# Performance work log

Measured on AMD Instinct MI355X. Metric: run time of the kernel, lower is better.

Reference implementation:

```python
import jax, jax.numpy as jnp
import numpy as np

DIM = 192
STATE = 64
B = 8
H = 64
W = 64
EPS_LN = 1e-5
EPS_BN = 1e-5


def _layernorm(x, g, b):
    m = jnp.mean(x, axis=-1, keepdims=True)
    v = jnp.mean((x - m) ** 2, axis=-1, keepdims=True)
    return (x - m) / jnp.sqrt(v + EPS_LN) * g + b


def _linear(x, w, b=None):
    # torch Linear convention: w is [out, in]
    y = jnp.einsum('...i,oi->...o', x, w)
    return y if b is None else y + b


def _parallel_scan(A, Bd, xp):
    # A, Bd, xp: [B, L, S]; h_t = A_t*h_{t-1} + Bd_t*xp_t via log-space cumsum
    A_safe = jnp.clip(A, 0.001, 0.999)
    log_A = jnp.log(A_safe + 1e-10)
    log_cum_A = jnp.cumsum(log_A, axis=1)
    log_cum_A_max = jnp.max(log_cum_A, axis=1, keepdims=True)
    cum_A = jnp.exp(log_cum_A - log_cum_A_max)
    BX = Bd * xp
    # prepend zeros, drop last: normalizer uses cumprod up to t-1
    log_pad = jnp.pad(log_cum_A - log_cum_A_max, ((0, 0), (1, 0), (0, 0)))[:, :-1]
    BX_norm = BX * jnp.exp(-log_pad)
    return jnp.cumsum(BX_norm, axis=1) * cum_A


def _ssm(x, ln_g, ln_b, xp_w, xp_b, dt_w, dt_b, A_log, B_w, C_w, Dp, out_w, out_b):
    xn = _layernorm(x, ln_g, ln_b)
    delta = jax.nn.softplus(_linear(xn, dt_w, dt_b)) * 0.01 + 0.0001  # [B,L,S]
    B_t = _linear(xn, B_w)
    C_t = _linear(xn, C_w)
    A = -jnp.exp(A_log)  # [S]
    x_proj = _linear(xn, xp_w, xp_b)
    deltaA = jnp.clip(delta * A, -10.0, -0.0001)
    A_disc = jnp.exp(deltaA)
    B_disc = delta * B_t
    h = _parallel_scan(A_disc, B_disc, x_proj)
    y = C_t * h
    y = jnp.where(jnp.all(jnp.isfinite(y)), y, jnp.zeros_like(y))
    y = _linear(y, out_w, out_b)
    return y + jnp.clip(Dp, -2.0, 2.0) * x


def reference(x, ln1_g, ln1_b, ln2_g, ln2_b, dw_w, bn_g, bn_b, bn_rm, bn_rv,
              ssm_ln_g, ssm_ln_b, xp_w, xp_b, dt_w, dt_b, A_log, B_w, C_w,
              D_param, out_w, out_b, mlp_w1, mlp_b1, mlp_w2, mlp_b2,
              alpha_local, alpha_ssm, alpha_mlp):
    identity = x
    # depthwise 3x3 conv + BatchNorm2d (eval mode, running stats)
    xc = jax.lax.conv_general_dilated(
        x, dw_w, (1, 1), 'SAME', feature_group_count=DIM,
        dimension_numbers=('NCHW', 'OIHW', 'NCHW'))
    scale = (bn_g / jnp.sqrt(bn_rv + EPS_BN))[None, :, None, None]
    x_local = (xc - bn_rm[None, :, None, None]) * scale + bn_b[None, :, None, None]
    # SSM branch on flattened spatial sequence
    x_seq = x.transpose(0, 2, 3, 1).reshape(B, H * W, DIM)
    x_seq = _layernorm(x_seq, ln1_g, ln1_b)
    x_seq = _ssm(x_seq, ssm_ln_g, ssm_ln_b, xp_w, xp_b, dt_w, dt_b, A_log,
                 B_w, C_w, D_param, out_w, out_b)
    x_ssm = x_seq.reshape(B, H, W, DIM).transpose(0, 3, 1, 2)
    xr = identity + alpha_local * x_local + alpha_ssm * x_ssm
    # residual MLP (dropout = identity at inference)
    x_mlp = xr.transpose(0, 2, 3, 1).reshape(B, H * W, DIM)
    x_mlp = _layernorm(x_mlp, ln2_g, ln2_b)
    x_mlp = _linear(jax.nn.gelu(_linear(x_mlp, mlp_w1, mlp_b1), approximate=False),
                    mlp_w2, mlp_b2)
    return xr + alpha_mlp * x_mlp.reshape(B, H, W, DIM).transpose(0, 3, 1, 2)


def setup_inputs() -> dict:
    key = jax.random.key(0)
    ks = jax.random.split(key, 12)
    def nrm(k, shape, s):
        return jax.random.normal(k, shape, jnp.float32) * s
    f32 = jnp.float32
    return {
        'x': jax.random.normal(ks[0], (B, DIM, H, W), f32),
        'ln1_g': jnp.ones(DIM, f32), 'ln1_b': jnp.zeros(DIM, f32),
        'ln2_g': jnp.ones(DIM, f32), 'ln2_b': jnp.zeros(DIM, f32),
        'dw_w': nrm(ks[1], (DIM, 1, 3, 3), 0.2),
        'bn_g': jnp.ones(DIM, f32), 'bn_b': jnp.zeros(DIM, f32),
        'bn_rm': jnp.zeros(DIM, f32), 'bn_rv': jnp.ones(DIM, f32),
        'ssm_ln_g': jnp.ones(DIM, f32), 'ssm_ln_b': jnp.zeros(DIM, f32),
        'xp_w': nrm(ks[2], (STATE, DIM), 0.05), 'xp_b': jnp.zeros(STATE, f32),
        'dt_w': nrm(ks[3], (STATE, DIM), 0.05), 'dt_b': jnp.zeros(STATE, f32),
        'A_log': jnp.log(jax.random.uniform(ks[4], (STATE,), f32) * 0.8 + 0.2),
        'B_w': nrm(ks[5], (STATE, DIM), 0.05),
        'C_w': nrm(ks[6], (STATE, DIM), 0.05),
        'D_param': jnp.zeros(DIM, f32),
        'out_w': nrm(ks[7], (DIM, STATE), 0.05), 'out_b': jnp.zeros(DIM, f32),
        'mlp_w1': nrm(ks[8], (4 * DIM, DIM), 0.03), 'mlp_b1': jnp.zeros(4 * DIM, f32),
        'mlp_w2': nrm(ks[9], (DIM, 4 * DIM), 0.03), 'mlp_b2': jnp.zeros(DIM, f32),
        'alpha_local': jnp.full((1,), 0.5, f32),
        'alpha_ssm': jnp.full((1,), 0.5, f32),
        'alpha_mlp': jnp.full((1,), 0.5, f32),
    }
```

## Files before the change

kernel.cpp:

```cpp
#include <hip/hip_runtime.h>
#include <hip/hip_bf16.h>
#include <math.h>


#define DEV static __device__ __forceinline__

constexpr int Bn = 8, Dm = 192, Ln = 4096, Sn = 64, Hd = 768;

typedef __attribute__((ext_vector_type(8))) short bf16x8;
typedef __attribute__((ext_vector_type(4))) float f32x4;

DEV float wave_sum(float v) {
#pragma unroll
  for (int off = 1; off < 64; off <<= 1) v += __shfl_xor(v, off);
  return v;
}

DEV short f2b(float x) {
  __hip_bfloat16 h = __float2bfloat16(x);
  return *(short*)&h;
}

DEV float b2f(short x) {
  __hip_bfloat16 h = *(__hip_bfloat16*)&x;
  return __bfloat162float(h);
}

__global__ __launch_bounds__(256) void k_prep(
    const float* __restrict__ x, const float* __restrict__ g1, const float* __restrict__ b1,
    const float* __restrict__ g2, const float* __restrict__ b2,
    short* __restrict__ xnb, short* __restrict__ xln1b,
    const float* __restrict__ dt_w, const float* __restrict__ B_w,
    const float* __restrict__ C_w, const float* __restrict__ xp_w,
    const float* __restrict__ out_w, const float* __restrict__ w1,
    const float* __restrict__ w2, short* __restrict__ wb) {
  __shared__ __align__(16) float tile[Dm * 65];
  int tid = threadIdx.x;
  if (blockIdx.y == 8) {
    for (int i = blockIdx.x * 256 + tid; i < 89088; i += 64 * 256) {
      const float4* src;
      if (i < 3072)       src = (const float4*)dt_w + i;
      else if (i < 6144)  src = (const float4*)B_w + (i - 3072);
      else if (i < 9216)  src = (const float4*)C_w + (i - 6144);
      else if (i < 12288) src = (const float4*)xp_w + (i - 9216);
      else if (i < 15360) src = (const float4*)out_w + (i - 12288);
      else if (i < 52224) src = (const float4*)w1 + (i - 15360);
      else                src = (const float4*)w2 + (i - 52224);
      float4 v = *src;
      int o = i * 4;
      wb[o] = f2b(v.x); wb[o + 1] = f2b(v.y); wb[o + 2] = f2b(v.z); wb[o + 3] = f2b(v.w);
    }
    return;
  }
  int b = blockIdx.y, l0 = blockIdx.x * 64;
  const float* xb = x + (size_t)b * Dm * Ln;
  for (int i = tid; i < Dm * 16; i += 256) {
    int d = i >> 4, l4 = (i & 15) << 2;
    float4 v = *(const float4*)&xb[d * Ln + l0 + l4];
    tile[d * 65 + l4]     = v.x; tile[d * 65 + l4 + 1] = v.y;
    tile[d * 65 + l4 + 2] = v.z; tile[d * 65 + l4 + 3] = v.w;
  }
  __syncthreads();
  int lane = tid & 63, wv = tid >> 6;
  float ga0 = g1[lane], ga1 = g1[lane + 64], ga2 = g1[lane + 128];
  float bb0 = b1[lane], bb1 = b1[lane + 64], bb2 = b1[lane + 128];
  float gc0 = g2[lane], gc1 = g2[lane + 64], gc2 = g2[lane + 128];
  float bc0 = b2[lane], bc1 = b2[lane + 64], bc2 = b2[lane + 128];
  for (int li = wv; li < 64; li += 4) {
    float v0 = tile[lane * 65 + li], v1 = tile[(lane + 64) * 65 + li], v2 = tile[(lane + 128) * 65 + li];
    float s  = wave_sum(v0 + v1 + v2);
    float sq = wave_sum(v0 * v0 + v1 * v1 + v2 * v2);
    float m = s * (1.f / 192.f);
    float inv = rsqrtf(sq * (1.f / 192.f) - m * m + 1e-5f);
    float y0 = (v0 - m) * inv * ga0 + bb0;
    float y1 = (v1 - m) * inv * ga1 + bb1;
    float y2 = (v2 - m) * inv * ga2 + bb2;
    float s2  = wave_sum(y0 + y1 + y2);
    float sq2 = wave_sum(y0 * y0 + y1 * y1 + y2 * y2);
    float m2 = s2 * (1.f / 192.f);
    float inv2 = rsqrtf(sq2 * (1.f / 192.f) - m2 * m2 + 1e-5f);
    size_t base = ((size_t)b * Ln + l0 + li) * Dm;
    xln1b[base + lane]       = f2b(y0);
    xln1b[base + lane + 64]  = f2b(y1);
    xln1b[base + lane + 128] = f2b(y2);
    xnb[base + lane]       = f2b((y0 - m2) * inv2 * gc0 + bc0);
    xnb[base + lane + 64]  = f2b((y1 - m2) * inv2 * gc1 + bc1);
    xnb[base + lane + 128] = f2b((y2 - m2) * inv2 * gc2 + bc2);
  }
}

__global__ __launch_bounds__(256) void k_proj(
    const short* __restrict__ xnb, const short* __restrict__ wcat,
    const float* __restrict__ dt_b, const float* __restrict__ xp_b,
    const float* __restrict__ A_log, float* __restrict__ aA, unsigned* __restrict__ bxc) {
  __shared__ __align__(16) short As[64 * 72];
  __shared__ __align__(16) short Bs[256 * 72];
  int m0 = blockIdx.x * 64, tid = threadIdx.x;
  int lane = tid & 63, l16 = lane & 15, quad = lane >> 4, w = tid >> 6;
  f32x4 acc[16] = {};
  for (int kt = 0; kt < 3; kt++) {
    int kb = kt * 64;
    for (int i = tid; i < 512; i += 256) {
      int row = i >> 3, c8 = (i & 7) * 8;
      *(float4*)&As[row * 72 + c8] = *(const float4*)&xnb[(size_t)(m0 + row) * 192 + kb + c8];
    }
    for (int i = tid; i < 2048; i += 256) {
      int row = i >> 3, c8 = (i & 7) * 8;
      *(float4*)&Bs[row * 72 + c8] = *(const float4*)&wcat[(size_t)row * 192 + kb + c8];
    }
    __syncthreads();
#pragma unroll
    for (int ks = 0; ks < 2; ks++) {
      int ko = ks * 32 + quad * 8;
      bf16x8 a0 = *(const bf16x8*)&As[(w * 16 + l16) * 72 + ko];
#pragma unroll
      for (int nh = 0; nh < 2; nh++) {
        bf16x8 bfr[8];
#pragma unroll
        for (int j = 0; j < 8; j++) bfr[j] = *(const bf16x8*)&Bs[((nh * 8 + j) * 16 + l16) * 72 + ko];
#pragma unroll
        for (int j = 0; j < 8; j++)
          acc[nh * 8 + j] = __builtin_amdgcn_mfma_f32_16x16x32_bf16(a0, bfr[j], acc[nh * 8 + j], 0, 0, 0);
      }
    }
    __syncthreads();
  }
  float Av[4], dtbv[4], xpbv[4];
#pragma unroll
  for (int ni = 0; ni < 4; ni++) {
    int s = ni * 16 + l16;
    Av[ni] = -expf(A_log[s]); dtbv[ni] = dt_b[s]; xpbv[ni] = xp_b[s];
  }
#pragma unroll
  for (int r = 0; r < 4; r++) {
    int m = m0 + w * 16 + quad * 4 + r;
#pragma unroll
    for (int ni = 0; ni < 4; ni++) {
      int s = ni * 16 + l16;
      float z = acc[ni][r] + dtbv[ni];
      float sp = (z > 20.f) ? z : log1pf(expf(z));
      float delta = sp * 0.01f + 0.0001f;
      float bt  = acc[ni + 4][r];
      float ct  = acc[ni + 8][r];
      float xpv = acc[ni + 12][r] + xpbv[ni];
      float dA = fminf(fmaxf(delta * Av[ni], -10.f), -0.0001f);
      float Ae = fminf(fmaxf(expf(dA), 0.001f), 0.999f) + 1e-10f;
      aA[(size_t)m * 64 + s] = Ae;
      unsigned pk = (unsigned)(unsigned short)f2b(delta * bt * xpv)
                  | ((unsigned)(unsigned short)f2b(ct) << 16);
      bxc[(size_t)m * 64 + s] = pk;
    }
  }
}

__global__ __launch_bounds__(64) void k_scan1(const float* __restrict__ aA,
                                              const unsigned* __restrict__ bxc,
                                              float* __restrict__ sums) {
  int c = blockIdx.x, b = blockIdx.y, s = threadIdx.x;
  size_t r0 = (size_t)b * Ln + c * 32;
  const float* ap = aA + r0 * 64;
  const unsigned* bp = bxc + r0 * 64;
  float prodA = 1.f, h = 0.f;
  int t = 0;
  if (c == 0) { prodA = ap[s]; h = b2f((short)(bp[s] & 0xFFFF)); t = 1; }
#pragma unroll 4
  for (; t < 32; t++) {
    float a = ap[t * 64 + s];
    float bx = b2f((short)(bp[t * 64 + s] & 0xFFFF));
    h = a * (h + bx);
    prodA *= a;
  }
  int ci = b * 128 + c;
  sums[(ci * 2 + 0) * 64 + s] = prodA;
  sums[(ci * 2 + 1) * 64 + s] = h;
}

__global__ __launch_bounds__(64) void k_scan2(const float* __restrict__ sums, float* __restrict__ carries) {
  int b = blockIdx.x, s = threadIdx.x;
  float cur = 0.f;
#pragma unroll 4
  for (int c = 0; c < 128; c++) {
    int ci = b * 128 + c;
    carries[ci * 64 + s] = cur;
    cur = sums[(ci * 2 + 0) * 64 + s] * cur + sums[(ci * 2 + 1) * 64 + s];
  }
}

__global__ __launch_bounds__(64) void k_scan3(const float* __restrict__ aA,
                                              const unsigned* __restrict__ bxc,
                                              const float* __restrict__ carries,
                                              short* __restrict__ y) {
  int c = blockIdx.x, b = blockIdx.y, s = threadIdx.x;
  size_t r0 = (size_t)b * Ln + c * 32;
  const float* ap = aA + r0 * 64;
  const unsigned* bp = bxc + r0 * 64;
  short* yo = y + r0 * 64;
  float h = carries[(b * 128 + c) * 64 + s];
  int t = 0;
  if (c == 0) {
    unsigned u = bp[s];
    h = b2f((short)(u & 0xFFFF));
    yo[s] = f2b(b2f((short)(u >> 16)) * h);
    t = 1;
  }
#pragma unroll 4
  for (; t < 32; t++) {
    unsigned u = bp[t * 64 + s];
    float a = ap[t * 64 + s];
    h = a * (h + b2f((short)(u & 0xFFFF)));
    yo[t * 64 + s] = f2b(b2f((short)(u >> 16)) * h);
  }
}

__global__ __launch_bounds__(256) void k_out(
    const short* __restrict__ y, const short* __restrict__ owb, const float* __restrict__ out_b,
    const float* __restrict__ Dp, const short* __restrict__ xln1b, float* __restrict__ sout) {
  __shared__ __align__(16) short As[96 * 72];
  __shared__ __align__(16) short Bs[64 * 72];
  int l0g = blockIdx.x * 64, d0 = blockIdx.y * 96, tid = threadIdx.x;
  int lane = tid & 63, l16 = lane & 15, quad = lane >> 4;
  int wm = (tid >> 6) >> 1, wn = (tid >> 6) & 1;
  f32x4 acc[3][2] = {};
  for (int i = tid; i < 768; i += 256) {
    int row = i >> 3, c8 = (i & 7) * 8;
    *(float4*)&As[row * 72 + c8] = *(const float4*)&owb[(d0 + row) * 64 + c8];
  }
  for (int i = tid; i < 512; i += 256) {
    int row = i >> 3, c8 = (i & 7) * 8;
    *(float4*)&Bs[row * 72 + c8] = *(const float4*)&y[(size_t)(l0g + row) * 64 + c8];
  }
  __syncthreads();
#pragma unroll
  for (int ks = 0; ks < 2; ks++) {
    int ko = ks * 32 + quad * 8;
    bf16x8 a[3], b[2];
#pragma unroll
    for (int mi = 0; mi < 3; mi++) a[mi] = *(const bf16x8*)&As[(wm * 48 + mi * 16 + l16) * 72 + ko];
#pragma unroll
    for (int ni = 0; ni < 2; ni++) b[ni] = *(const bf16x8*)&Bs[(wn * 32 + ni * 16 + l16) * 72 + ko];
#pragma unroll
    for (int mi = 0; mi < 3; mi++)
#pragma unroll
      for (int ni = 0; ni < 2; ni++)
        acc[mi][ni] = __builtin_amdgcn_mfma_f32_16x16x32_bf16(a[mi], b[ni], acc[mi][ni], 0, 0, 0);
  }
  int bb = l0g >> 12;
#pragma unroll
  for (int mi = 0; mi < 3; mi++)
#pragma unroll
    for (int r = 0; r < 4; r++) {
      int d = d0 + wm * 48 + mi * 16 + quad * 4 + r;
      float ob = out_b[d];
      float dc = fminf(fmaxf(Dp[d], -2.f), 2.f);
#pragma unroll
      for (int ni = 0; ni < 2; ni++) {
        int l = l0g + wn * 32 + ni * 16 + l16;
        float v = acc[mi][ni][r] + ob;
        if (dc != 0.f) v += dc * b2f(xln1b[(size_t)l * 192 + d]);
        sout[((size_t)bb * Dm + d) * Ln + (l & 4095)] = v;
      }
    }
}

__global__ __launch_bounds__(256) void k_conv(
    const float* __restrict__ x, const float* __restrict__ dw,
    const float* __restrict__ bn_g, const float* __restrict__ bn_b,
    const float* __restrict__ bn_rm, const float* __restrict__ bn_rv,
    const float* __restrict__ sout, const float* __restrict__ a_loc,
    const float* __restrict__ a_ssm, float* __restrict__ xr) {
  __shared__ __align__(16) float xs[64 * 64];
  int d = blockIdx.x, b = blockIdx.y, tid = threadIdx.x;
  const float* xp = x + ((size_t)b * Dm + d) * Ln;
  for (int i = tid; i < 1024; i += 256) ((float4*)xs)[i] = ((const float4*)xp)[i];
  __syncthreads();
  float w[9];
#pragma unroll
  for (int k = 0; k < 9; k++) w[k] = dw[d * 9 + k];
  float scale = bn_g[d] * rsqrtf(bn_rv[d] + 1e-5f);
  float rm = bn_rm[d], bb = bn_b[d];
  float al = a_loc[0], as_ = a_ssm[0];
  const float* sp = sout + ((size_t)b * Dm + d) * Ln;
  float* xo = xr + ((size_t)b * Dm + d) * Ln;
  for (int i = tid; i < 4096; i += 256) {
    int h = i >> 6, wc = i & 63;
    float acc = 0.f;
#pragma unroll
    for (int kh = 0; kh < 3; kh++) {
      int hh = h + kh - 1;
      if (hh < 0 || hh >= 64) continue;
#pragma unroll
      for (int kw = 0; kw < 3; kw++) {
        int ww2 = wc + kw - 1;
        if (ww2 < 0 || ww2 >= 64) continue;
        acc += xs[hh * 64 + ww2] * w[kh * 3 + kw];
      }
    }
    float xl = (acc - rm) * scale + bb;
    xo[i] = xs[i] + al * xl + as_ * sp[i];
  }
}

__global__ __launch_bounds__(256) void k_ln2(
    const float* __restrict__ xr, const float* __restrict__ g, const float* __restrict__ bb,
    short* __restrict__ xn2) {
  __shared__ __align__(16) float tile[Dm * 65];
  int b = blockIdx.y, l0 = blockIdx.x * 64, tid = threadIdx.x;
  const float* xb = xr + (size_t)b * Dm * Ln;
  for (int i = tid; i < Dm * 16; i += 256) {
    int d = i >> 4, l4 = (i & 15) << 2;
    float4 v = *(const float4*)&xb[d * Ln + l0 + l4];
    tile[d * 65 + l4]     = v.x; tile[d * 65 + l4 + 1] = v.y;
    tile[d * 65 + l4 + 2] = v.z; tile[d * 65 + l4 + 3] = v.w;
  }
  __syncthreads();
  int lane = tid & 63, wv = tid >> 6;
  float g0 = g[lane], g1v = g[lane + 64], g2v = g[lane + 128];
  float b0 = bb[lane], b1v = bb[lane + 64], b2v = bb[lane + 128];
  for (int li = wv; li < 64; li += 4) {
    float v0 = tile[lane * 65 + li], v1 = tile[(lane + 64) * 65 + li], v2 = tile[(lane + 128) * 65 + li];
    float s  = wave_sum(v0 + v1 + v2);
    float sq = wave_sum(v0 * v0 + v1 * v1 + v2 * v2);
    float m = s * (1.f / 192.f);
    float inv = rsqrtf(sq * (1.f / 192.f) - m * m + 1e-5f);
    size_t base = ((size_t)b * Ln + l0 + li) * Dm;
    xn2[base + lane]       = f2b((v0 - m) * inv * g0 + b0);
    xn2[base + lane + 64]  = f2b((v1 - m) * inv * g1v + b1v);
    xn2[base + lane + 128] = f2b((v2 - m) * inv * g2v + b2v);
  }
}

__global__ __launch_bounds__(256) void k_gemm1(
    const short* __restrict__ xn2, const short* __restrict__ w1b,
    const float* __restrict__ b1h, short* __restrict__ hid) {
  __shared__ __align__(16) short smem[2 * 128 * 88];
  short* As = smem;
  short* Bs = smem + 128 * 88;
  int m0 = blockIdx.x * 128, n0 = blockIdx.y * 128, tid = threadIdx.x;
  int lane = tid & 63, l16 = lane & 15, quad = lane >> 4;
  int wm = (tid >> 6) >> 1, wn = (tid >> 6) & 1;
  f32x4 acc[4][4] = {};
  for (int kt = 0; kt < 3; kt++) {
    int kb = kt * 64;
    for (int i = tid; i < 1024; i += 256) {
      int row = i >> 3, c8 = (i & 7) * 8;
      *(float4*)&As[row * 88 + c8] = *(const float4*)&xn2[(size_t)(m0 + row) * 192 + kb + c8];
      *(float4*)&Bs[row * 88 + c8] = *(const float4*)&w1b[(size_t)(n0 + row) * 192 + kb + c8];
    }
    __syncthreads();
#pragma unroll
    for (int ks = 0; ks < 2; ks++) {
      int ko = ks * 32 + quad * 8;
      bf16x8 a[4], b[4];
#pragma unroll
      for (int mi = 0; mi < 4; mi++) a[mi] = *(const bf16x8*)&As[(wm * 64 + mi * 16 + l16) * 88 + ko];
#pragma unroll
      for (int ni = 0; ni < 4; ni++) b[ni] = *(const bf16x8*)&Bs[(wn * 64 + ni * 16 + l16) * 88 + ko];
#pragma unroll
      for (int mi = 0; mi < 4; mi++)
#pragma unroll
        for (int ni = 0; ni < 4; ni++)
          acc[mi][ni] = __builtin_amdgcn_mfma_f32_16x16x32_bf16(a[mi], b[ni], acc[mi][ni], 0, 0, 0);
    }
    __syncthreads();
  }
  short* Cs = smem;
  float bias4[4];
#pragma unroll
  for (int ni = 0; ni < 4; ni++) bias4[ni] = b1h[n0 + wn * 64 + ni * 16 + l16];
#pragma unroll
  for (int mi = 0; mi < 4; mi++)
#pragma unroll
    for (int ni = 0; ni < 4; ni++) {
      int n = wn * 64 + ni * 16 + l16;
#pragma unroll
      for (int r = 0; r < 4; r++) {
        int m = wm * 64 + mi * 16 + quad * 4 + r;
        float v = acc[mi][ni][r] + bias4[ni];
        float g = 0.5f * v * (1.f + erff(v * 0.70710678118f));
        Cs[m * 136 + n] = f2b(g);
      }
    }
  __syncthreads();
  for (int i = tid; i < 2048; i += 256) {
    int m = i >> 4, ch = i & 15;
    *(float4*)&hid[(size_t)(m0 + m) * 768 + n0 + ch * 8] = *(const float4*)&Cs[m * 136 + ch * 8];
  }
}

__global__ __launch_bounds__(256) void k_gemm2(
    const short* __restrict__ hid, const short* __restrict__ w2b,
    const float* __restrict__ b2o, const float* __restrict__ xr,
    const float* __restrict__ am, float* __restrict__ out) {
  __shared__ __align__(16) short Wt[96 * 88];
  __shared__ __align__(16) short Ht[64 * 88];
  int l0g = blockIdx.x * 64, d0 = blockIdx.y * 96, tid = threadIdx.x;
  int lane = tid & 63, l16 = lane & 15, quad = lane >> 4;
  int wm = (tid >> 6) >> 1, wn = (tid >> 6) & 1;
  f32x4 acc[3][2] = {};
  for (int kt = 0; kt < 12; kt++) {
    int kb = kt * 64;
    for (int i = tid; i < 768; i += 256) {
      int row = i >> 3, c8 = (i & 7) * 8;
      *(float4*)&Wt[row * 88 + c8] = *(const float4*)&w2b[(size_t)(d0 + row) * 768 + kb + c8];
    }
    for (int i = tid; i < 512; i += 256) {
      int row = i >> 3, c8 = (i & 7) * 8;
      *(float4*)&Ht[row * 88 + c8] = *(const float4*)&hid[(size_t)(l0g + row) * 768 + kb + c8];
    }
    __syncthreads();
#pragma unroll
    for (int ks = 0; ks < 2; ks++) {
      int ko = ks * 32 + quad * 8;
      bf16x8 a[3], b[2];
#pragma unroll
      for (int mi = 0; mi < 3; mi++) a[mi] = *(const bf16x8*)&Wt[(wm * 48 + mi * 16 + l16) * 88 + ko];
#pragma unroll
      for (int ni = 0; ni < 2; ni++) b[ni] = *(const bf16x8*)&Ht[(wn * 32 + ni * 16 + l16) * 88 + ko];
#pragma unroll
      for (int mi = 0; mi < 3; mi++)
#pragma unroll
        for (int ni = 0; ni < 2; ni++)
          acc[mi][ni] = __builtin_amdgcn_mfma_f32_16x16x32_bf16(a[mi], b[ni], acc[mi][ni], 0, 0, 0);
    }
    __syncthreads();
  }
  float alpha = am[0];
#pragma unroll
  for (int mi = 0; mi < 3; mi++)
#pragma unroll
    for (int r = 0; r < 4; r++) {
      int d = d0 + wm * 48 + mi * 16 + quad * 4 + r;
      float bias = b2o[d];
#pragma unroll
      for (int ni = 0; ni < 2; ni++) {
        int lg = l0g + wn * 32 + ni * 16 + l16;
        size_t idx = ((size_t)(lg >> 12) * Dm + d) * Ln + (lg & 4095);
        out[idx] = xr[idx] + alpha * (acc[mi][ni][r] + bias);
      }
    }
}

extern "C" void kernel_launch(void* const* d_in, const int* in_sizes, int n_in,
                              void* d_out, int out_size, void* d_ws, size_t ws_size,
                              hipStream_t stream) {
  (void)in_sizes; (void)n_in; (void)out_size; (void)ws_size;
  const float* x     = (const float*)d_in[0];
  const float* ln1_g = (const float*)d_in[1];
  const float* ln1_b = (const float*)d_in[2];
  const float* ln2_g = (const float*)d_in[3];
  const float* ln2_b = (const float*)d_in[4];
  const float* dw_w  = (const float*)d_in[5];
  const float* bn_g  = (const float*)d_in[6];
  const float* bn_b  = (const float*)d_in[7];
  const float* bn_rm = (const float*)d_in[8];
  const float* bn_rv = (const float*)d_in[9];
  const float* ssm_g = (const float*)d_in[10];
  const float* ssm_b = (const float*)d_in[11];
  const float* xp_w  = (const float*)d_in[12];
  const float* xp_b  = (const float*)d_in[13];
  const float* dt_w  = (const float*)d_in[14];
  const float* dt_b  = (const float*)d_in[15];
  const float* A_log = (const float*)d_in[16];
  const float* B_w   = (const float*)d_in[17];
  const float* C_w   = (const float*)d_in[18];
  const float* Dp    = (const float*)d_in[19];
  const float* out_w = (const float*)d_in[20];
  const float* out_b = (const float*)d_in[21];
  const float* w1    = (const float*)d_in[22];
  const float* b1    = (const float*)d_in[23];
  const float* w2    = (const float*)d_in[24];
  const float* b2    = (const float*)d_in[25];
  const float* a_loc = (const float*)d_in[26];
  const float* a_ssm = (const float*)d_in[27];
  const float* a_mlp = (const float*)d_in[28];

  float* ws = (float*)d_ws;
  short*    xnb   = (short*)ws;
  short*    xln1b = (short*)(ws + 3145728);
  float*    aA    = ws + 6291456;
  unsigned* bxc   = (unsigned*)(ws + 8388608);
  short*    yB    = (short*)(ws + 10485760);
  float*    sout  = ws + 11534336;
  float*    xr    = ws + 17825792;
  short*    wb    = (short*)(ws + 24117248);
  float*    sums  = ws + 24829952;
  float*    carr  = ws + 24961024;
  short*    xn2   = (short*)(ws + 25026560);
  short*    hid   = (short*)(ws + 28172288);
  short*    wcatb = wb;
  short*    owb   = wb + 49152;
  short*    w1b   = wb + 61440;
  short*    w2b   = wb + 208896;
  float*    out   = (float*)d_out;

  k_prep <<<dim3(64, 9),  256, 0, stream>>>(x, ln1_g, ln1_b, ssm_g, ssm_b, xnb, xln1b,
                                            dt_w, B_w, C_w, xp_w, out_w, w1, w2, wb);
  k_proj <<<dim3(512),    256, 0, stream>>>(xnb, wcatb, dt_b, xp_b, A_log, aA, bxc);
  k_scan1<<<dim3(128, 8),  64, 0, stream>>>(aA, bxc, sums);
  k_scan2<<<dim3(8),       64, 0, stream>>>(sums, carr);
  k_scan3<<<dim3(128, 8),  64, 0, stream>>>(aA, bxc, carr, yB);
  k_out  <<<dim3(512, 2), 256, 0, stream>>>(yB, owb, out_b, Dp, xln1b, sout);
  k_conv <<<dim3(192, 8), 256, 0, stream>>>(x, dw_w, bn_g, bn_b, bn_rm, bn_rv, sout, a_loc, a_ssm, xr);
  k_ln2  <<<dim3(64, 8),  256, 0, stream>>>(xr, ln2_g, ln2_b, xn2);
  k_gemm1<<<dim3(256, 6), 256, 0, stream>>>(xn2, w1b, b1, hid);
  k_gemm2<<<dim3(512, 2), 256, 0, stream>>>(hid, w2b, b2, xr, a_mlp, out);
}
```

Baseline: 290.2 us.

## Fuse SSM output projection with depthwise conv and residual combine

Merges the out-projection GEMM kernel and the depthwise conv/BN/residual kernel into one kernel. After the MFMA tile, each block stages a 3-row halo of x (bf16) plus per-channel conv/BN parameters in shared memory, computes the conv per output element, and writes xr directly. This removes the fp32 sout intermediate round-trip and one launch. It adds bf16 rounding of the conv input and scattered strided x reads, and the larger shared footprint may lower occupancy.

After: 307.9 us. 6.1% more time.

```diff
diff --git a/kernel.cpp b/kernel.cpp
--- a/kernel.cpp
+++ b/kernel.cpp
@@ -212,12 +212,21 @@
   }
 }
 
-__global__ __launch_bounds__(256) void k_out(
+__global__ __launch_bounds__(256) void k_outconv(
     const short* __restrict__ y, const short* __restrict__ owb, const float* __restrict__ out_b,
-    const float* __restrict__ Dp, const short* __restrict__ xln1b, float* __restrict__ sout) {
-  __shared__ __align__(16) short As[96 * 72];
-  __shared__ __align__(16) short Bs[64 * 72];
+    const float* __restrict__ Dp, const short* __restrict__ xln1b,
+    const float* __restrict__ x, const float* __restrict__ dw,
+    const float* __restrict__ bn_g, const float* __restrict__ bn_b,
+    const float* __restrict__ bn_rm, const float* __restrict__ bn_rv,
+    const float* __restrict__ a_loc, const float* __restrict__ a_ssm,
+    float* __restrict__ xr) {
+  __shared__ __align__(16) short smem[22080];
+  short* As = smem;
+  short* Bs = smem + 6912;
+  short* xl = smem;
+  float* prm = (float*)(smem + 19008);
   int l0g = blockIdx.x * 64, d0 = blockIdx.y * 96, tid = threadIdx.x;
+  int b = l0g >> 12, h = (l0g >> 6) & 63;
   int lane = tid & 63, l16 = lane & 15, quad = lane >> 4;
   int wm = (tid >> 6) >> 1, wn = (tid >> 6) & 1;
   f32x4 acc[3][2] = {};
@@ -233,71 +242,70 @@
 #pragma unroll
   for (int ks = 0; ks < 2; ks++) {
     int ko = ks * 32 + quad * 8;
-    bf16x8 a[3], b[2];
+    bf16x8 a[3], bfr[2];
 #pragma unroll
     for (int mi = 0; mi < 3; mi++) a[mi] = *(const bf16x8*)&As[(wm * 48 + mi * 16 + l16) * 72 + ko];
 #pragma unroll
-    for (int ni = 0; ni < 2; ni++) b[ni] = *(const bf16x8*)&Bs[(wn * 32 + ni * 16 + l16) * 72 + ko];
+    for (int ni = 0; ni < 2; ni++) bfr[ni] = *(const bf16x8*)&Bs[(wn * 32 + ni * 16 + l16) * 72 + ko];
 #pragma unroll
     for (int mi = 0; mi < 3; mi++)
 #pragma unroll
       for (int ni = 0; ni < 2; ni++)
-        acc[mi][ni] = __builtin_amdgcn_mfma_f32_16x16x32_bf16(a[mi], b[ni], acc[mi][ni], 0, 0, 0);
-  }
-  int bb = l0g >> 12;
+        acc[mi][ni] = __builtin_amdgcn_mfma_f32_16x16x32_bf16(a[mi], bfr[ni], acc[mi][ni], 0, 0, 0);
+  }
+  __syncthreads();
+  for (int i = tid; i < 4608; i += 256) {
+    int rr = i / 1536, rem = i % 1536;
+    int d = rem >> 4, w4 = (rem & 15) * 4;
+    int hh = h - 1 + rr;
+    float4 v = make_float4(0.f, 0.f, 0.f, 0.f);
+    if (hh >= 0 && hh < 64)
+      v = *(const float4*)&x[((size_t)b * Dm + d0 + d) * Ln + hh * 64 + w4];
+    int o = rr * 6336 + d * 66 + 1 + w4;
+    xl[o] = f2b(v.x); xl[o + 1] = f2b(v.y); xl[o + 2] = f2b(v.z); xl[o + 3] = f2b(v.w);
+  }
+  for (int i = tid; i < 288; i += 256) {
+    int rr = i / 96, d = i % 96;
+    xl[rr * 6336 + d * 66] = 0;
+    xl[rr * 6336 + d * 66 + 65] = 0;
+  }
+  if (tid < 96) {
+    int d = d0 + tid;
+    float* p = prm + tid * 16;
+#pragma unroll
+    for (int j = 0; j < 9; j++) p[j] = dw[d * 9 + j];
+    float sc = bn_g[d] * rsqrtf(bn_rv[d] + 1e-5f);
+    p[9] = sc;
+    p[10] = bn_b[d] - bn_rm[d] * sc;
+    p[11] = fminf(fmaxf(Dp[d], -2.f), 2.f);
+    p[12] = out_b[d];
+  }
+  __syncthreads();
+  float al = a_loc[0], as_ = a_ssm[0];
 #pragma unroll
   for (int mi = 0; mi < 3; mi++)
 #pragma unroll
     for (int r = 0; r < 4; r++) {
-      int d = d0 + wm * 48 + mi * 16 + quad * 4 + r;
-      float ob = out_b[d];
-      float dc = fminf(fmaxf(Dp[d], -2.f), 2.f);
+      int dl = wm * 48 + mi * 16 + quad * 4 + r;
+      int d = d0 + dl;
+      const float* p = prm + dl * 16;
+      float sc = p[9], sh = p[10], dcD = p[11], ob = p[12];
 #pragma unroll
       for (int ni = 0; ni < 2; ni++) {
-        int l = l0g + wn * 32 + ni * 16 + l16;
+        int w = wn * 32 + ni * 16 + l16;
+        float cacc = 0.f;
+#pragma unroll
+        for (int rr = 0; rr < 3; rr++)
+#pragma unroll
+          for (int ww = 0; ww < 3; ww++)
+            cacc += b2f(xl[rr * 6336 + dl * 66 + w + ww]) * p[rr * 3 + ww];
+        float x_local = cacc * sc + sh;
         float v = acc[mi][ni][r] + ob;
-        if (dc != 0.f) v += dc * b2f(xln1b[(size_t)l * 192 + d]);
-        sout[((size_t)bb * Dm + d) * Ln + (l & 4095)] = v;
+        if (dcD != 0.f) v += dcD * b2f(xln1b[(size_t)(l0g + w) * 192 + d]);
+        size_t idx = ((size_t)b * Dm + d) * Ln + h * 64 + w;
+        xr[idx] = x[idx] + al * x_local + as_ * v;
       }
     }
-}
-
-__global__ __launch_bounds__(256) void k_conv(
-    const float* __restrict__ x, const float* __restrict__ dw,
-    const float* __restrict__ bn_g, const float* __restrict__ bn_b,
-    const float* __restrict__ bn_rm, const float* __restrict__ bn_rv,
-    const float* __restrict__ sout, const float* __restrict__ a_loc,
-    const float* __restrict__ a_ssm, float* __restrict__ xr) {
-  __shared__ __align__(16) float xs[64 * 64];
-  int d = blockIdx.x, b = blockIdx.y, tid = threadIdx.x;
-  const float* xp = x + ((size_t)b * Dm + d) * Ln;
-  for (int i = tid; i < 1024; i += 256) ((float4*)xs)[i] = ((const float4*)xp)[i];
-  __syncthreads();
-  float w[9];
-#pragma unroll
-  for (int k = 0; k < 9; k++) w[k] = dw[d * 9 + k];
-  float scale = bn_g[d] * rsqrtf(bn_rv[d] + 1e-5f);
-  float rm = bn_rm[d], bb = bn_b[d];
-  float al = a_loc[0], as_ = a_ssm[0];
-  const float* sp = sout + ((size_t)b * Dm + d) * Ln;
-  float* xo = xr + ((size_t)b * Dm + d) * Ln;
-  for (int i = tid; i < 4096; i += 256) {
-    int h = i >> 6, wc = i & 63;
-    float acc = 0.f;
-#pragma unroll
-    for (int kh = 0; kh < 3; kh++) {
-      int hh = h + kh - 1;
-      if (hh < 0 || hh >= 64) continue;
-#pragma unroll
-      for (int kw = 0; kw < 3; kw++) {
-        int ww2 = wc + kw - 1;
-        if (ww2 < 0 || ww2 >= 64) continue;
-        acc += xs[hh * 64 + ww2] * w[kh * 3 + kw];
-      }
-    }
-    float xl = (acc - rm) * scale + bb;
-    xo[i] = xs[i] + al * xl + as_ * sp[i];
-  }
 }
 
 __global__ __launch_bounds__(256) void k_ln2(
@@ -480,7 +488,6 @@
   float*    aA    = ws + 6291456;
   unsigned* bxc   = (unsigned*)(ws + 8388608);
   short*    yB    = (short*)(ws + 10485760);
-  float*    sout  = ws + 11534336;
   float*    xr    = ws + 17825792;
   short*    wb    = (short*)(ws + 24117248);
   float*    sums  = ws + 24829952;
@@ -493,15 +500,16 @@
   short*    w2b   = wb + 208896;
   float*    out   = (float*)d_out;
 
-  k_prep <<<dim3(64, 9),  256, 0, stream>>>(x, ln1_g, ln1_b, ssm_g, ssm_b, xnb, xln1b,
-                                            dt_w, B_w, C_w, xp_w, out_w, w1, w2, wb);
-  k_proj <<<dim3(512),    256, 0, stream>>>(xnb, wcatb, dt_b, xp_b, A_log, aA, bxc);
-  k_scan1<<<dim3(128, 8),  64, 0, stream>>>(aA, bxc, sums);
-  k_scan2<<<dim3(8),       64, 0, stream>>>(sums, carr);
-  k_scan3<<<dim3(128, 8),  64, 0, stream>>>(aA, bxc, carr, yB);
-  k_out  <<<dim3(512, 2), 256, 0, stream>>>(yB, owb, out_b, Dp, xln1b, sout);
-  k_conv <<<dim3(192, 8), 256, 0, stream>>>(x, dw_w, bn_g, bn_b, bn_rm, bn_rv, sout, a_loc, a_ssm, xr);
-  k_ln2  <<<dim3(64, 8),  256, 0, stream>>>(xr, ln2_g, ln2_b, xn2);
-  k_gemm1<<<dim3(256, 6), 256, 0, stream>>>(xn2, w1b, b1, hid);
-  k_gemm2<<<dim3(512, 2), 256, 0, stream>>>(hid, w2b, b2, xr, a_mlp, out);
-}
+  k_prep   <<<dim3(64, 9),  256, 0, stream>>>(x, ln1_g, ln1_b, ssm_g, ssm_b, xnb, xln1b,
+                                              dt_w, B_w, C_w, xp_w, out_w, w1, w2, wb);
+  k_proj   <<<dim3(512),    256, 0, stream>>>(xnb, wcatb, dt_b, xp_b, A_log, aA, bxc);
+  k_scan1  <<<dim3(128, 8),  64, 0, stream>>>(aA, bxc, sums);
+  k_scan2  <<<dim3(8),       64, 0, stream>>>(sums, carr);
+  k_scan3  <<<dim3(128, 8),  64, 0, stream>>>(aA, bxc, carr, yB);
+  k_outconv<<<dim3(512, 2), 256, 0, stream>>>(yB, owb, out_b, Dp, xln1b,
+                                              x, dw_w, bn_g, bn_b, bn_rm, bn_rv,
+                                              a_loc, a_ssm, xr);
+  k_ln2    <<<dim3(64, 8),  256, 0, stream>>>(xr, ln2_g, ln2_b, xn2);
+  k_gemm1  <<<dim3(256, 6), 256, 0, stream>>>(xn2, w1b, b1, hid);
+  k_gemm2  <<<dim3(512, 2), 256, 0, stream>>>(hid, w2b, b2, xr, a_mlp, out);
+}
```
